# Optimization experiments

Hardware: AMD Instinct MI355X
Metric: run time of the kernel (lower is better)

## Reference

```python
import jax, jax.numpy as jnp
import numpy as np

HEADS = 8
DIM_HEAD = 64
LN_EPS = 1e-5


def rotate_half(x):
    # pairs (x0,x1) -> (-x1,x0), interleaved layout (einops '(d r)' with r=2)
    x1 = x[..., 0::2]
    x2 = x[..., 1::2]
    return jnp.stack((-x2, x1), axis=-1).reshape(x.shape)


def apply_rope(freqs, x):
    return x * jnp.cos(freqs) + rotate_half(x) * jnp.sin(freqs)


def setup_inputs() -> dict:
    key = jax.random.key(0)
    ks = jax.random.split(key, 4)
    b, n, dim = 2, 4096, 512
    inner = HEADS * DIM_HEAD
    x = jax.random.normal(ks[0], (b, n, dim), dtype=jnp.float32)
    rotary_time_emb = jax.random.uniform(ks[1], (b, n, DIM_HEAD), jnp.float32, 0.0, 6.283185)
    ln_w = jnp.ones((dim,), jnp.float32)
    ln_b = jnp.zeros((dim,), jnp.float32)
    w_qkv = jax.random.normal(ks[2], (inner * 3, dim), jnp.float32) * (dim ** -0.5)
    w_out = jax.random.normal(ks[3], (dim, inner), jnp.float32) * (inner ** -0.5)
    b_out = jnp.zeros((dim,), jnp.float32)
    return dict(x=x, rotary_time_emb=rotary_time_emb, ln_w=ln_w, ln_b=ln_b,
                w_qkv=w_qkv, w_out=w_out, b_out=b_out)


def reference(x, rotary_time_emb, ln_w, ln_b, w_qkv, w_out, b_out):
    b, n, dim = x.shape
    # LayerNorm
    mu = jnp.mean(x, axis=-1, keepdims=True)
    var = jnp.var(x, axis=-1, keepdims=True)
    xn = (x - mu) * jax.lax.rsqrt(var + LN_EPS) * ln_w + ln_b
    # QKV projection (Linear, no bias)
    qkv = xn @ w_qkv.T  # [b, n, 3*inner]
    q, k, v = jnp.split(qkv, 3, axis=-1)

    def to_heads(t):
        return t.reshape(b, n, HEADS, DIM_HEAD).transpose(0, 2, 1, 3)  # b h n d

    q, k, v = to_heads(q), to_heads(k), to_heads(v)
    freqs = rotary_time_emb[:, None, :, :]  # b 1 n d, broadcast over heads
    q = apply_rope(freqs, q)
    k = apply_rope(freqs, k)
    v = apply_rope(freqs, v)  # rotate_value=True
    scale = jnp.asarray(DIM_HEAD ** -0.5, dtype=x.dtype)
    scores = jnp.einsum('bhqd,bhkd->bhqk', q, k) * scale
    attn = jax.nn.softmax(scores, axis=-1)
    out = jnp.einsum('bhqk,bhkd->bhqd', attn, v)
    out = apply_rope(-freqs, out)  # inverse rotation of the output
    out = out.transpose(0, 2, 1, 3).reshape(b, n, HEADS * DIM_HEAD)
    return out @ w_out.T + b_out
```

## Files before the change

### kernel.cpp

```cpp
#include <hip/hip_runtime.h>
#include <cmath>

typedef short bf16x8 __attribute__((ext_vector_type(8)));
typedef float f32x2 __attribute__((ext_vector_type(2)));
typedef float f32x4 __attribute__((ext_vector_type(4)));
typedef float f32x16 __attribute__((ext_vector_type(16)));

#define NSEQ 4096
#define BATCH 2
#define DIM 512
#define HEADS 8
#define NROWS (BATCH * NSEQ)
#define QKVN (3 * DIM)

__device__ __forceinline__ unsigned short f2bf(float f) {
  unsigned int u = __float_as_uint(f);
  u += 0x7fffu + ((u >> 16) & 1u);
  return (unsigned short)(u >> 16);
}
__device__ __forceinline__ float bf2f(unsigned short h) {
  return __uint_as_float(((unsigned int)h) << 16);
}
__device__ __forceinline__ void gload16(const unsigned short* g, unsigned short* l) {
  __builtin_amdgcn_global_load_lds((const __attribute__((address_space(1))) unsigned int*)g,
                                   (__attribute__((address_space(3))) unsigned int*)l, 16, 0, 0);
}

__global__ __launch_bounds__(256) void k_tables(const float* __restrict__ rot,
                                                float* __restrict__ cosT,
                                                float* __restrict__ sinT) {
  int i = blockIdx.x * 256 + threadIdx.x;
  float f = rot[i];
  cosT[i] = cosf(f);
  sinT[i] = sinf(f);
}

__global__ __launch_bounds__(256) void k_cvt(const float* __restrict__ src,
                                             unsigned short* __restrict__ dst, int n) {
  int i = blockIdx.x * 256 + threadIdx.x;
  if (i < n) dst[i] = f2bf(src[i]);
}

__global__ __launch_bounds__(256) void k_ln(const float* __restrict__ x,
                                            const float* __restrict__ w,
                                            const float* __restrict__ bb,
                                            unsigned short* __restrict__ xn) {
  int row = blockIdx.x * 4 + (threadIdx.x >> 6);
  int lane = threadIdx.x & 63;
  const float* xr = x + (size_t)row * DIM;
  float v[8];
  float s = 0.f;
#pragma unroll
  for (int j = 0; j < 8; ++j) { v[j] = xr[lane + j * 64]; s += v[j]; }
#pragma unroll
  for (int m = 1; m < 64; m <<= 1) s += __shfl_xor(s, m);
  float mu = s * (1.0f / DIM);
  float q = 0.f;
#pragma unroll
  for (int j = 0; j < 8; ++j) { float d = v[j] - mu; q += d * d; }
#pragma unroll
  for (int m = 1; m < 64; m <<= 1) q += __shfl_xor(q, m);
  float rs = rsqrtf(q * (1.0f / DIM) + 1e-5f);
#pragma unroll
  for (int j = 0; j < 8; ++j) {
    int col = lane + j * 64;
    xn[(size_t)row * DIM + col] = f2bf((v[j] - mu) * rs * w[col] + bb[col]);
  }
}

template <int EPI>
__global__ __launch_bounds__(256) void k_gemm(const unsigned short* __restrict__ A,
                                              const unsigned short* __restrict__ B,
                                              void* __restrict__ C,
                                              const float* __restrict__ bias,
                                              int M, int N, int K) {
  __shared__ __align__(16) unsigned short As[2][128 * 32];
  __shared__ __align__(16) unsigned short Bs[2][128 * 32];
  int bm = blockIdx.x, bn = blockIdx.y;
  int tid = threadIdx.x;
  int lane = tid & 63, w = tid >> 6;
  int wm = (w >> 1) << 6, wn = (w & 1) << 6;
  f32x4 acc[4][4] = {};

#define GSTAGE(KT, BUF) do { \
  _Pragma("unroll") \
  for (int i = 0; i < 2; ++i) { \
    int c = tid + (i << 8); \
    int row = c >> 2, kc = (c & 3) << 3; \
    gload16(A + (size_t)(bm * 128 + row) * K + (KT) + kc, &As[BUF][(w * 64 + i * 256) * 8]); \
    gload16(B + (size_t)(bn * 128 + row) * K + (KT) + kc, &Bs[BUF][(w * 64 + i * 256) * 8]); \
  } } while (0)

  GSTAGE(0, 0);
  __syncthreads();
  int nk = K >> 5;
  for (int t = 0; t < nk; ++t) {
    int cur = t & 1;
    if (t + 1 < nk) GSTAGE((t + 1) << 5, cur ^ 1);
    bf16x8 af[4], bfr[4];
#pragma unroll
    for (int mi = 0; mi < 4; ++mi)
      af[mi] = *(const bf16x8*)&As[cur][(wm + mi * 16 + (lane & 15)) * 32 + ((lane >> 4) << 3)];
#pragma unroll
    for (int ni = 0; ni < 4; ++ni)
      bfr[ni] = *(const bf16x8*)&Bs[cur][(wn + ni * 16 + (lane & 15)) * 32 + ((lane >> 4) << 3)];
#pragma unroll
    for (int mi = 0; mi < 4; ++mi)
#pragma unroll
      for (int ni = 0; ni < 4; ++ni)
        acc[mi][ni] = __builtin_amdgcn_mfma_f32_16x16x32_bf16(af[mi], bfr[ni], acc[mi][ni], 0, 0, 0);
    __syncthreads();
  }
#undef GSTAGE
#pragma unroll
  for (int mi = 0; mi < 4; ++mi) {
#pragma unroll
    for (int ni = 0; ni < 4; ++ni) {
#pragma unroll
      for (int r = 0; r < 4; ++r) {
        int gm = bm * 128 + wm + mi * 16 + ((lane >> 4) << 2) + r;
        int gn = bn * 128 + wn + ni * 16 + (lane & 15);
        if (EPI == 0) {
          ((unsigned short*)C)[(size_t)gm * N + gn] = f2bf(acc[mi][ni][r]);
        } else {
          ((float*)C)[(size_t)gm * N + gn] = acc[mi][ni][r] + bias[gn];
        }
      }
    }
  }
}

__global__ __launch_bounds__(256) void k_rope_split(const unsigned short* __restrict__ qkv,
                                                    const float* __restrict__ cosT,
                                                    const float* __restrict__ sinT,
                                                    unsigned short* __restrict__ qh,
                                                    unsigned short* __restrict__ kh,
                                                    unsigned short* __restrict__ vt) {
  __shared__ unsigned short vs[128][65];
  const float QSC = 0.125f * 1.44269504f;
  int nt = blockIdx.x, bh = blockIdx.y;
  int b = bh >> 3, h = bh & 7;
  int n0 = nt * 128;
  int t = threadIdx.x;
  int sub = t >> 3, cc = t & 7;
#pragma unroll
  for (int rr = 0; rr < 4; ++rr) {
    int row = rr * 32 + sub;
    int n = n0 + row;
    size_t base = ((size_t)(b * NSEQ + n)) * QKVN + h * 64 + cc * 8;
    const float* cb = cosT + ((size_t)(b * NSEQ + n)) * 64 + cc * 8;
    const float* sb = sinT + ((size_t)(b * NSEQ + n)) * 64 + cc * 8;
    float c[8], sn[8];
#pragma unroll
    for (int j = 0; j < 8; ++j) { c[j] = cb[j]; sn[j] = sb[j]; }
    bf16x8 qv = *(const bf16x8*)(qkv + base);
    bf16x8 kv = *(const bf16x8*)(qkv + base + 512);
    bf16x8 vv = *(const bf16x8*)(qkv + base + 1024);
    union { bf16x8 v; unsigned short u[8]; } yq, yk;
#pragma unroll
    for (int j = 0; j < 8; j += 2) {
      {
        float e = bf2f((unsigned short)qv[j]), o = bf2f((unsigned short)qv[j + 1]);
        yq.u[j]     = f2bf((e * c[j] - o * sn[j]) * QSC);
        yq.u[j + 1] = f2bf((o * c[j + 1] + e * sn[j + 1]) * QSC);
      }
      {
        float e = bf2f((unsigned short)kv[j]), o = bf2f((unsigned short)kv[j + 1]);
        yk.u[j]     = f2bf(e * c[j] - o * sn[j]);
        yk.u[j + 1] = f2bf(o * c[j + 1] + e * sn[j + 1]);
      }
      {
        float e = bf2f((unsigned short)vv[j]), o = bf2f((unsigned short)vv[j + 1]);
        vs[row][cc * 8 + j]     = f2bf(e * c[j] - o * sn[j]);
        vs[row][cc * 8 + j + 1] = f2bf(o * c[j + 1] + e * sn[j + 1]);
      }
    }
    *(bf16x8*)(qh + ((size_t)bh * NSEQ + n) * 64 + cc * 8) = yq.v;
    *(bf16x8*)(kh + ((size_t)bh * NSEQ + n) * 64 + cc * 8) = yk.v;
  }
  __syncthreads();
  int d = t >> 2, c4 = t & 3;
#pragma unroll
  for (int g = 0; g < 4; ++g) {
    union { bf16x8 v; unsigned short u[8]; } tv;
#pragma unroll
    for (int j = 0; j < 8; ++j) tv.u[j] = vs[c4 * 32 + g * 8 + j][d];
    *(bf16x8*)(vt + ((size_t)bh * 64 + d) * NSEQ + n0 + c4 * 32 + g * 8) = tv.v;
  }
}

__global__ __launch_bounds__(256, 4) void k_attn(const unsigned short* __restrict__ Qh,
                                                 const unsigned short* __restrict__ Kh,
                                                 const unsigned short* __restrict__ VT,
                                                 float* __restrict__ opart,
                                                 float* __restrict__ lpart) {
  __shared__ __align__(16) unsigned short Ks[2][64 * 64];
  __shared__ __align__(16) unsigned short Vs[2][64 * 64];
  int bid = blockIdx.x;
  int bh   = (bid & 7) + 8 * ((bid >> 8) & 1);
  int qt   = (bid >> 3) & 31;
  int half = bid >> 9;
  int tid = threadIdx.x;
  int w = tid >> 6, lane = tid & 63;
  int lq = lane & 31, hi = lane >> 5;
  int q0 = qt * 128 + w * 32;
  int kv0 = half * 2048;

  const unsigned short* Kbh = Kh + (size_t)bh * NSEQ * 64;
  const unsigned short* Vbh = VT + (size_t)bh * 64 * NSEQ;

  const unsigned short* Qb = Qh + ((size_t)bh * NSEQ + q0 + lq) * 64 + hi * 8;
  bf16x8 qf[4];
#pragma unroll
  for (int j = 0; j < 4; ++j) qf[j] = *(const bf16x8*)(Qb + j * 16);

  int c0 = w * 64 + lane;
  int r0 = c0 >> 3, sw0 = ((c0 & 7) ^ (r0 & 7)) << 3;
  int c1 = c0 + 256;
  int r1 = c1 >> 3, sw1 = ((c1 & 7) ^ (r1 & 7)) << 3;
  int ld0 = (w * 64) * 8, ld1 = (256 + w * 64) * 8;

  f32x16 acc0 = (f32x16)0.0f, acc1 = (f32x16)0.0f;
  float l_run = 0.f;
  int swz = (lq & 7) << 4;

  gload16(Kbh + ((size_t)kv0 + r0) * 64 + sw0, &Ks[0][ld0]);
  gload16(Kbh + ((size_t)kv0 + r1) * 64 + sw1, &Ks[0][ld1]);
  gload16(Vbh + (size_t)r0 * NSEQ + kv0 + sw0, &Vs[0][ld0]);
  gload16(Vbh + (size_t)r1 * NSEQ + kv0 + sw1, &Vs[0][ld1]);
  __syncthreads();

#define PHASE(PH) do { \
  f32x16 s = (f32x16)0.0f; \
  __builtin_amdgcn_s_setprio(1); \
  _Pragma("unroll") \
  for (int j = 0; j < 4; ++j) { \
    int cb = j * 32 + hi * 16; \
    bf16x8 a = *(const bf16x8*)(kb_ + ((PH) * 32 + lq) * 128 + (cb ^ swz)); \
    s = __builtin_amdgcn_mfma_f32_32x32x16_bf16(a, qf[j], s, 0, 0, 0); \
  } \
  __builtin_amdgcn_s_setprio(0); \
  _Pragma("unroll") \
  for (int r = 0; r < 16; ++r) s[r] = __builtin_amdgcn_exp2f(s[r]); \
  union { f32x16 v; f32x2 p[8]; } su; su.v = s; \
  f32x2 t01 = su.p[0] + su.p[1], t23 = su.p[2] + su.p[3]; \
  f32x2 t45 = su.p[4] + su.p[5], t67 = su.p[6] + su.p[7]; \
  f32x2 tt = (t01 + t23) + (t45 + t67); \
  l_run += tt.x + tt.y; \
  unsigned int dw[8], xw[8]; \
  _Pragma("unroll") \
  for (int m = 0; m < 8; ++m) \
    asm("v_cvt_pk_bf16_f32 %0, %1, %2" : "=v"(dw[m]) : "v"(s[2 * m]), "v"(s[2 * m + 1])); \
  _Pragma("unroll") \
  for (int m = 0; m < 8; ++m) xw[m] = (unsigned int)__shfl_xor((int)dw[m], 32); \
  __builtin_amdgcn_s_setprio(1); \
  _Pragma("unroll") \
  for (int kk = 0; kk < 2; ++kk) { \
    const int B = 4 * kk; \
    union { unsigned int d[4]; bf16x8 v; } pu; \
    pu.d[0] = hi ? xw[B + 2] : dw[B + 0]; \
    pu.d[1] = hi ? xw[B + 3] : dw[B + 1]; \
    pu.d[2] = hi ? dw[B + 2] : xw[B + 0]; \
    pu.d[3] = hi ? dw[B + 3] : xw[B + 1]; \
    int cb = ((PH) * 2 + kk) * 32 + hi * 16; \
    bf16x8 v0 = *(const bf16x8*)(vb_ + lq * 128 + (cb ^ swz)); \
    bf16x8 v1 = *(const bf16x8*)(vb_ + (32 + lq) * 128 + (cb ^ swz)); \
    acc0 = __builtin_amdgcn_mfma_f32_32x32x16_bf16(v0, pu.v, acc0, 0, 0, 0); \
    acc1 = __builtin_amdgcn_mfma_f32_32x32x16_bf16(v1, pu.v, acc1, 0, 0, 0); \
  } \
  __builtin_amdgcn_s_setprio(0); \
} while (0)

#define TILE(T, CUR) do { \
  if ((T) < 31) { \
    int tg = kv0 + ((T) + 1) * 64; \
    gload16(Kbh + ((size_t)tg + r0) * 64 + sw0, &Ks[(CUR) ^ 1][ld0]); \
    gload16(Kbh + ((size_t)tg + r1) * 64 + sw1, &Ks[(CUR) ^ 1][ld1]); \
    gload16(Vbh + (size_t)r0 * NSEQ + tg + sw0, &Vs[(CUR) ^ 1][ld0]); \
    gload16(Vbh + (size_t)r1 * NSEQ + tg + sw1, &Vs[(CUR) ^ 1][ld1]); \
  } \
  const char* kb_ = (const char*)&Ks[CUR][0]; \
  const char* vb_ = (const char*)&Vs[CUR][0]; \
  PHASE(0); \
  PHASE(1); \
  __syncthreads(); \
} while (0)

  for (int tp = 0; tp < 16; ++tp) {
    TILE(2 * tp, 0);
    TILE(2 * tp + 1, 1);
  }
#undef TILE
#undef PHASE

  float lsum = l_run + __shfl_xor(l_run, 32);
  size_t qrow = (size_t)(half * 16 + bh) * NSEQ + q0 + lq;
  if (hi == 0) lpart[qrow] = lsum;
  float* ob = opart + qrow * 64;
#pragma unroll
  for (int rg = 0; rg < 4; ++rg) {
    float4 v0 = make_float4(acc0[4 * rg + 0], acc0[4 * rg + 1], acc0[4 * rg + 2], acc0[4 * rg + 3]);
    float4 v1 = make_float4(acc1[4 * rg + 0], acc1[4 * rg + 1], acc1[4 * rg + 2], acc1[4 * rg + 3]);
    *(float4*)(ob + 8 * rg + 4 * hi) = v0;
    *(float4*)(ob + 32 + 8 * rg + 4 * hi) = v1;
  }
}

__global__ __launch_bounds__(256) void k_combine(const float* __restrict__ opart,
                                                 const float* __restrict__ lpart,
                                                 const float* __restrict__ cosT,
                                                 const float* __restrict__ sinT,
                                                 unsigned short* __restrict__ ao) {
  int bh = blockIdx.y;
  int b = bh >> 3, h = bh & 7;
  int t = threadIdx.x;
  int q = blockIdx.x * 16 + (t >> 4);
  int d = (t & 15) * 4;
  size_t i0 = (size_t)bh * NSEQ + q;
  const size_t HOFF = (size_t)16 * NSEQ;
  float4 o0 = *(const float4*)(opart + i0 * 64 + d);
  float4 o1 = *(const float4*)(opart + (i0 + HOFF) * 64 + d);
  float inv = 1.0f / (lpart[i0] + lpart[i0 + HOFF]);
  float4 c4 = *(const float4*)(cosT + ((size_t)b * NSEQ + q) * 64 + d);
  float4 s4 = *(const float4*)(sinT + ((size_t)b * NSEQ + q) * 64 + d);
  float yx = (o0.x + o1.x) * inv;
  float yy = (o0.y + o1.y) * inv;
  float yz = (o0.z + o1.z) * inv;
  float yw = (o0.w + o1.w) * inv;
  float r0 = yx * c4.x + yy * s4.x;
  float r1 = yy * c4.y - yx * s4.y;
  float r2 = yz * c4.z + yw * s4.z;
  float r3 = yw * c4.w - yz * s4.w;
  unsigned int w0, w1;
  asm("v_cvt_pk_bf16_f32 %0, %1, %2" : "=v"(w0) : "v"(r0), "v"(r1));
  asm("v_cvt_pk_bf16_f32 %0, %1, %2" : "=v"(w1) : "v"(r2), "v"(r3));
  unsigned int uu[2] = {w0, w1};
  *(uint2*)(ao + ((size_t)b * NSEQ + q) * DIM + h * 64 + d) = *(uint2*)uu;
}

extern "C" void kernel_launch(void* const* d_in, const int* in_sizes, int n_in,
                              void* d_out, int out_size, void* d_ws, size_t ws_size,
                              hipStream_t stream) {
  const float* x    = (const float*)d_in[0];
  const float* rot  = (const float*)d_in[1];
  const float* lnw  = (const float*)d_in[2];
  const float* lnb  = (const float*)d_in[3];
  const float* wqkv = (const float*)d_in[4];
  const float* wout = (const float*)d_in[5];
  const float* bout = (const float*)d_in[6];
  float* out = (float*)d_out;

  char* ws = (char*)d_ws;
  const size_t MB = (size_t)1 << 20;
  float* cosT          = (float*)(ws + 0 * MB);
  float* sinT          = (float*)(ws + 2 * MB);
  unsigned short* wqkb = (unsigned short*)(ws + 4 * MB);
  float* lpart         = (float*)(ws + 5 * MB + 512 * 1024);
  unsigned short* wob  = (unsigned short*)(ws + 6 * MB);
  unsigned short* xn   = (unsigned short*)(ws + 8 * MB);
  float* opart         = (float*)(ws + 8 * MB);
  unsigned short* qkv  = (unsigned short*)(ws + 16 * MB);
  unsigned short* qh   = (unsigned short*)(ws + 40 * MB);
  unsigned short* ao   = (unsigned short*)(ws + 40 * MB);
  unsigned short* kh   = (unsigned short*)(ws + 48 * MB);
  unsigned short* vt   = (unsigned short*)(ws + 56 * MB);

  k_tables<<<(BATCH * NSEQ * 64) / 256, 256, 0, stream>>>(rot, cosT, sinT);
  k_cvt<<<(QKVN * DIM + 255) / 256, 256, 0, stream>>>(wqkv, wqkb, QKVN * DIM);
  k_cvt<<<(DIM * DIM + 255) / 256, 256, 0, stream>>>(wout, wob, DIM * DIM);
  k_ln<<<NROWS / 4, 256, 0, stream>>>(x, lnw, lnb, xn);
  k_gemm<0><<<dim3(NROWS / 128, QKVN / 128), 256, 0, stream>>>(xn, wqkb, qkv, nullptr,
                                                               NROWS, QKVN, DIM);
  k_rope_split<<<dim3(NSEQ / 128, 16), 256, 0, stream>>>(qkv, cosT, sinT, qh, kh, vt);
  k_attn<<<1024, 256, 0, stream>>>(qh, kh, vt, opart, lpart);
  k_combine<<<dim3(NSEQ / 16, 16), 256, 0, stream>>>(opart, lpart, cosT, sinT, ao);
  k_gemm<1><<<dim3(NROWS / 128, DIM / 128), 256, 0, stream>>>(ao, wob, out, bout,
                                                              NROWS, DIM, DIM);
}
```

Measured before the change: 157.1 us.

## Process two 32-row query tiles per wave in attention to reuse K/V fragments

Each wave in the attention kernel now handles 64 query rows (two 32-row MFMA tiles) instead of 32, so every K and V fragment read from LDS feeds twice as many MFMAs. The block count halves to 512 and the occupancy hint drops from 4 to 2 blocks per CU. The P-fragment exchange also changes: it now shuffles only the half each lane needs rather than all eight words. The aim is to cut LDS read traffic and K/V global loads per unit of work. The cost is higher register pressure and fewer resident waves to hide latency.

```diff
diff --git a/kernel.cpp b/kernel.cpp
--- a/kernel.cpp
+++ b/kernel.cpp
@@ -189,7 +189,7 @@
   }
 }
 
-__global__ __launch_bounds__(256, 4) void k_attn(const unsigned short* __restrict__ Qh,
+__global__ __launch_bounds__(256, 2) void k_attn(const unsigned short* __restrict__ Qh,
                                                  const unsigned short* __restrict__ Kh,
                                                  const unsigned short* __restrict__ VT,
                                                  float* __restrict__ opart,
@@ -197,22 +197,26 @@
   __shared__ __align__(16) unsigned short Ks[2][64 * 64];
   __shared__ __align__(16) unsigned short Vs[2][64 * 64];
   int bid = blockIdx.x;
-  int bh   = (bid & 7) + 8 * ((bid >> 8) & 1);
-  int qt   = (bid >> 3) & 31;
-  int half = bid >> 9;
+  int bh   = (bid & 7) + 8 * ((bid >> 7) & 1);
+  int qt   = (bid >> 3) & 15;
+  int half = (bid >> 8) & 1;
   int tid = threadIdx.x;
   int w = tid >> 6, lane = tid & 63;
   int lq = lane & 31, hi = lane >> 5;
-  int q0 = qt * 128 + w * 32;
+  int q0 = qt * 256 + w * 64;
   int kv0 = half * 2048;
 
   const unsigned short* Kbh = Kh + (size_t)bh * NSEQ * 64;
   const unsigned short* Vbh = VT + (size_t)bh * 64 * NSEQ;
 
-  const unsigned short* Qb = Qh + ((size_t)bh * NSEQ + q0 + lq) * 64 + hi * 8;
-  bf16x8 qf[4];
-#pragma unroll
-  for (int j = 0; j < 4; ++j) qf[j] = *(const bf16x8*)(Qb + j * 16);
+  const unsigned short* QbA = Qh + ((size_t)bh * NSEQ + q0 + lq) * 64 + hi * 8;
+  const unsigned short* QbB = QbA + 32 * 64;
+  bf16x8 qfA[4], qfB[4];
+#pragma unroll
+  for (int j = 0; j < 4; ++j) {
+    qfA[j] = *(const bf16x8*)(QbA + j * 16);
+    qfB[j] = *(const bf16x8*)(QbB + j * 16);
+  }
 
   int c0 = w * 64 + lane;
   int r0 = c0 >> 3, sw0 = ((c0 & 7) ^ (r0 & 7)) << 3;
@@ -220,8 +224,9 @@
   int r1 = c1 >> 3, sw1 = ((c1 & 7) ^ (r1 & 7)) << 3;
   int ld0 = (w * 64) * 8, ld1 = (256 + w * 64) * 8;
 
-  f32x16 acc0 = (f32x16)0.0f, acc1 = (f32x16)0.0f;
-  float l_run = 0.f;
+  f32x16 accA0 = (f32x16)0.0f, accA1 = (f32x16)0.0f;
+  f32x16 accB0 = (f32x16)0.0f, accB1 = (f32x16)0.0f;
+  float lA = 0.f, lB = 0.f;
   int swz = (lq & 7) << 4;
 
   gload16(Kbh + ((size_t)kv0 + r0) * 64 + sw0, &Ks[0][ld0]);
@@ -230,79 +235,104 @@
   gload16(Vbh + (size_t)r1 * NSEQ + kv0 + sw1, &Vs[0][ld1]);
   __syncthreads();
 
-#define PHASE(PH) do { \
-  f32x16 s = (f32x16)0.0f; \
-  __builtin_amdgcn_s_setprio(1); \
-  _Pragma("unroll") \
-  for (int j = 0; j < 4; ++j) { \
-    int cb = j * 32 + hi * 16; \
-    bf16x8 a = *(const bf16x8*)(kb_ + ((PH) * 32 + lq) * 128 + (cb ^ swz)); \
-    s = __builtin_amdgcn_mfma_f32_32x32x16_bf16(a, qf[j], s, 0, 0, 0); \
-  } \
-  __builtin_amdgcn_s_setprio(0); \
-  _Pragma("unroll") \
-  for (int r = 0; r < 16; ++r) s[r] = __builtin_amdgcn_exp2f(s[r]); \
-  union { f32x16 v; f32x2 p[8]; } su; su.v = s; \
-  f32x2 t01 = su.p[0] + su.p[1], t23 = su.p[2] + su.p[3]; \
-  f32x2 t45 = su.p[4] + su.p[5], t67 = su.p[6] + su.p[7]; \
-  f32x2 tt = (t01 + t23) + (t45 + t67); \
-  l_run += tt.x + tt.y; \
-  unsigned int dw[8], xw[8]; \
-  _Pragma("unroll") \
-  for (int m = 0; m < 8; ++m) \
-    asm("v_cvt_pk_bf16_f32 %0, %1, %2" : "=v"(dw[m]) : "v"(s[2 * m]), "v"(s[2 * m + 1])); \
-  _Pragma("unroll") \
-  for (int m = 0; m < 8; ++m) xw[m] = (unsigned int)__shfl_xor((int)dw[m], 32); \
-  __builtin_amdgcn_s_setprio(1); \
-  _Pragma("unroll") \
-  for (int kk = 0; kk < 2; ++kk) { \
-    const int B = 4 * kk; \
-    union { unsigned int d[4]; bf16x8 v; } pu; \
-    pu.d[0] = hi ? xw[B + 2] : dw[B + 0]; \
-    pu.d[1] = hi ? xw[B + 3] : dw[B + 1]; \
-    pu.d[2] = hi ? dw[B + 2] : xw[B + 0]; \
-    pu.d[3] = hi ? dw[B + 3] : xw[B + 1]; \
-    int cb = ((PH) * 2 + kk) * 32 + hi * 16; \
-    bf16x8 v0 = *(const bf16x8*)(vb_ + lq * 128 + (cb ^ swz)); \
-    bf16x8 v1 = *(const bf16x8*)(vb_ + (32 + lq) * 128 + (cb ^ swz)); \
-    acc0 = __builtin_amdgcn_mfma_f32_32x32x16_bf16(v0, pu.v, acc0, 0, 0, 0); \
-    acc1 = __builtin_amdgcn_mfma_f32_32x32x16_bf16(v1, pu.v, acc1, 0, 0, 0); \
-  } \
-  __builtin_amdgcn_s_setprio(0); \
-} while (0)
-
-#define TILE(T, CUR) do { \
-  if ((T) < 31) { \
-    int tg = kv0 + ((T) + 1) * 64; \
-    gload16(Kbh + ((size_t)tg + r0) * 64 + sw0, &Ks[(CUR) ^ 1][ld0]); \
-    gload16(Kbh + ((size_t)tg + r1) * 64 + sw1, &Ks[(CUR) ^ 1][ld1]); \
-    gload16(Vbh + (size_t)r0 * NSEQ + tg + sw0, &Vs[(CUR) ^ 1][ld0]); \
-    gload16(Vbh + (size_t)r1 * NSEQ + tg + sw1, &Vs[(CUR) ^ 1][ld1]); \
-  } \
-  const char* kb_ = (const char*)&Ks[CUR][0]; \
-  const char* vb_ = (const char*)&Vs[CUR][0]; \
-  PHASE(0); \
-  PHASE(1); \
-  __syncthreads(); \
-} while (0)
-
-  for (int tp = 0; tp < 16; ++tp) {
-    TILE(2 * tp, 0);
-    TILE(2 * tp + 1, 1);
-  }
-#undef TILE
-#undef PHASE
-
-  float lsum = l_run + __shfl_xor(l_run, 32);
-  size_t qrow = (size_t)(half * 16 + bh) * NSEQ + q0 + lq;
-  if (hi == 0) lpart[qrow] = lsum;
-  float* ob = opart + qrow * 64;
+  for (int t = 0; t < 32; ++t) {
+    int cur = t & 1;
+    if (t < 31) {
+      int tg = kv0 + (t + 1) * 64;
+      gload16(Kbh + ((size_t)tg + r0) * 64 + sw0, &Ks[cur ^ 1][ld0]);
+      gload16(Kbh + ((size_t)tg + r1) * 64 + sw1, &Ks[cur ^ 1][ld1]);
+      gload16(Vbh + (size_t)r0 * NSEQ + tg + sw0, &Vs[cur ^ 1][ld0]);
+      gload16(Vbh + (size_t)r1 * NSEQ + tg + sw1, &Vs[cur ^ 1][ld1]);
+    }
+    const char* kb_ = (const char*)&Ks[cur][0];
+    const char* vb_ = (const char*)&Vs[cur][0];
+#pragma unroll
+    for (int ph = 0; ph < 2; ++ph) {
+      f32x16 sA = (f32x16)0.0f, sB = (f32x16)0.0f;
+      __builtin_amdgcn_s_setprio(1);
+#pragma unroll
+      for (int j = 0; j < 4; ++j) {
+        int cb = j * 32 + hi * 16;
+        bf16x8 a = *(const bf16x8*)(kb_ + (ph * 32 + lq) * 128 + (cb ^ swz));
+        sA = __builtin_amdgcn_mfma_f32_32x32x16_bf16(a, qfA[j], sA, 0, 0, 0);
+        sB = __builtin_amdgcn_mfma_f32_32x32x16_bf16(a, qfB[j], sB, 0, 0, 0);
+      }
+      __builtin_amdgcn_s_setprio(0);
+#pragma unroll
+      for (int r = 0; r < 16; ++r) sA[r] = __builtin_amdgcn_exp2f(sA[r]);
+#pragma unroll
+      for (int r = 0; r < 16; ++r) sB[r] = __builtin_amdgcn_exp2f(sB[r]);
+      {
+        union { f32x16 v; f32x2 p[8]; } ua, ub; ua.v = sA; ub.v = sB;
+        f32x2 a01 = ua.p[0] + ua.p[1], a23 = ua.p[2] + ua.p[3];
+        f32x2 a45 = ua.p[4] + ua.p[5], a67 = ua.p[6] + ua.p[7];
+        f32x2 ta = (a01 + a23) + (a45 + a67);
+        lA += ta.x + ta.y;
+        f32x2 b01 = ub.p[0] + ub.p[1], b23 = ub.p[2] + ub.p[3];
+        f32x2 b45 = ub.p[4] + ub.p[5], b67 = ub.p[6] + ub.p[7];
+        f32x2 tb = (b01 + b23) + (b45 + b67);
+        lB += tb.x + tb.y;
+      }
+      unsigned int dwA[8], dwB[8];
+#pragma unroll
+      for (int m = 0; m < 8; ++m) {
+        asm("v_cvt_pk_bf16_f32 %0, %1, %2" : "=v"(dwA[m]) : "v"(sA[2 * m]), "v"(sA[2 * m + 1]));
+        asm("v_cvt_pk_bf16_f32 %0, %1, %2" : "=v"(dwB[m]) : "v"(sB[2 * m]), "v"(sB[2 * m + 1]));
+      }
+      __builtin_amdgcn_s_setprio(1);
+#pragma unroll
+      for (int kk = 0; kk < 2; ++kk) {
+        const int B = 4 * kk;
+        unsigned int svA0 = hi ? dwA[B + 0] : dwA[B + 2];
+        unsigned int svA1 = hi ? dwA[B + 1] : dwA[B + 3];
+        unsigned int svB0 = hi ? dwB[B + 0] : dwB[B + 2];
+        unsigned int svB1 = hi ? dwB[B + 1] : dwB[B + 3];
+        unsigned int rvA0 = (unsigned int)__shfl_xor((int)svA0, 32);
+        unsigned int rvA1 = (unsigned int)__shfl_xor((int)svA1, 32);
+        unsigned int rvB0 = (unsigned int)__shfl_xor((int)svB0, 32);
+        unsigned int rvB1 = (unsigned int)__shfl_xor((int)svB1, 32);
+        union { unsigned int d[4]; bf16x8 v; } puA, puB;
+        puA.d[0] = hi ? rvA0 : dwA[B + 0];
+        puA.d[1] = hi ? rvA1 : dwA[B + 1];
+        puA.d[2] = hi ? dwA[B + 2] : rvA0;
+        puA.d[3] = hi ? dwA[B + 3] : rvA1;
+        puB.d[0] = hi ? rvB0 : dwB[B + 0];
+        puB.d[1] = hi ? rvB1 : dwB[B + 1];
+        puB.d[2] = hi ? dwB[B + 2] : rvB0;
+        puB.d[3] = hi ? dwB[B + 3] : rvB1;
+        int cb = (ph * 2 + kk) * 32 + hi * 16;
+        bf16x8 v0 = *(const bf16x8*)(vb_ + lq * 128 + (cb ^ swz));
+        bf16x8 v1 = *(const bf16x8*)(vb_ + (32 + lq) * 128 + (cb ^ swz));
+        accA0 = __builtin_amdgcn_mfma_f32_32x32x16_bf16(v0, puA.v, accA0, 0, 0, 0);
+        accA1 = __builtin_amdgcn_mfma_f32_32x32x16_bf16(v1, puA.v, accA1, 0, 0, 0);
+        accB0 = __builtin_amdgcn_mfma_f32_32x32x16_bf16(v0, puB.v, accB0, 0, 0, 0);
+        accB1 = __builtin_amdgcn_mfma_f32_32x32x16_bf16(v1, puB.v, accB1, 0, 0, 0);
+      }
+      __builtin_amdgcn_s_setprio(0);
+    }
+    __syncthreads();
+  }
+
+  float lsumA = lA + __shfl_xor(lA, 32);
+  float lsumB = lB + __shfl_xor(lB, 32);
+  size_t qrowA = (size_t)(half * 16 + bh) * NSEQ + q0 + lq;
+  size_t qrowB = qrowA + 32;
+  if (hi == 0) {
+    lpart[qrowA] = lsumA;
+    lpart[qrowB] = lsumB;
+  }
+  float* obA = opart + qrowA * 64;
+  float* obB = opart + qrowB * 64;
 #pragma unroll
   for (int rg = 0; rg < 4; ++rg) {
-    float4 v0 = make_float4(acc0[4 * rg + 0], acc0[4 * rg + 1], acc0[4 * rg + 2], acc0[4 * rg + 3]);
-    float4 v1 = make_float4(acc1[4 * rg + 0], acc1[4 * rg + 1], acc1[4 * rg + 2], acc1[4 * rg + 3]);
-    *(float4*)(ob + 8 * rg + 4 * hi) = v0;
-    *(float4*)(ob + 32 + 8 * rg + 4 * hi) = v1;
+    float4 a0 = make_float4(accA0[4 * rg + 0], accA0[4 * rg + 1], accA0[4 * rg + 2], accA0[4 * rg + 3]);
+    float4 a1 = make_float4(accA1[4 * rg + 0], accA1[4 * rg + 1], accA1[4 * rg + 2], accA1[4 * rg + 3]);
+    float4 b0 = make_float4(accB0[4 * rg + 0], accB0[4 * rg + 1], accB0[4 * rg + 2], accB0[4 * rg + 3]);
+    float4 b1 = make_float4(accB1[4 * rg + 0], accB1[4 * rg + 1], accB1[4 * rg + 2], accB1[4 * rg + 3]);
+    *(float4*)(obA + 8 * rg + 4 * hi) = a0;
+    *(float4*)(obA + 32 + 8 * rg + 4 * hi) = a1;
+    *(float4*)(obB + 8 * rg + 4 * hi) = b0;
+    *(float4*)(obB + 32 + 8 * rg + 4 * hi) = b1;
   }
 }
 
@@ -372,7 +402,7 @@
   k_gemm<0><<<dim3(NROWS / 128, QKVN / 128), 256, 0, stream>>>(xn, wqkb, qkv, nullptr,
                                                                NROWS, QKVN, DIM);
   k_rope_split<<<dim3(NSEQ / 128, 16), 256, 0, stream>>>(qkv, cosT, sinT, qh, kh, vt);
-  k_attn<<<1024, 256, 0, stream>>>(qh, kh, vt, opart, lpart);
+  k_attn<<<512, 256, 0, stream>>>(qh, kh, vt, opart, lpart);
   k_combine<<<dim3(NSEQ / 16, 16), 256, 0, stream>>>(opart, lpart, cosT, sinT, ao);
   k_gemm<1><<<dim3(NROWS / 128, DIM / 128), 256, 0, stream>>>(ao, wob, out, bout,
                                                               NROWS, DIM, DIM);
```

New measurement: 148.1 us. 1.06x faster.
